# Kernel tuning notes

Measured on AMD Instinct MI355X. Metric: run time of the kernel, lower is better.

Reference implementation:

```python
import jax, jax.numpy as jnp
import numpy as np

B, T, DIM, H, D = 4, 2048, 1024, 8, 128
HDIM = H * D


def _rope_tables(t, head_dim):
    # angular_freq: (1/1024)^linspace(0,1,D/4) concatenated with D/4 zeros -> length D/2
    freq = (1.0 / 1024.0) ** jnp.linspace(0.0, 1.0, head_dim // 4)
    freq = jnp.concatenate([freq.astype(jnp.float32), jnp.zeros(head_dim // 4, jnp.float32)])
    theta = jnp.arange(t, dtype=jnp.float32)[:, None] * freq[None, :]  # [T, D/2]
    return jnp.cos(theta), jnp.sin(theta)


def _rms_norm(x):
    # F.rms_norm with no weight, default eps = finfo(dtype).eps
    eps = jnp.finfo(jnp.float32).eps
    return x * jax.lax.rsqrt(jnp.mean(x * x, axis=-1, keepdims=True) + eps)


def _rope(x, cos, sin):
    # x: [B,T,H,D]; rotate-half form matching the torch module
    x1, x2 = jnp.split(x, 2, axis=-1)
    c = cos[None, :, None, :]
    s = sin[None, :, None, :]
    return jnp.concatenate([x1 * c + x2 * s, -x1 * s + x2 * c], axis=-1)


def setup_inputs() -> dict:
    key = jax.random.key(0)
    k0, k1, k2, k3 = jax.random.split(key, 4)
    std = 0.5 * DIM ** -0.5
    bound = (3.0 ** 0.5) * std
    x = jax.random.normal(k0, (B, T, DIM), jnp.float32)
    ve = jax.random.normal(k1, (B, T, HDIM), jnp.float32)
    qkv_w = jax.random.uniform(k2, (3, HDIM, DIM), jnp.float32, -bound, bound)
    lambdas = jnp.array([0.5, 0.5], jnp.float32)
    # c_proj is zero-initialized in the module; use small random weight so output is nontrivial
    c_proj_w = jax.random.uniform(k3, (DIM, HDIM), jnp.float32, -bound, bound)
    return {"x": x, "ve": ve, "qkv_w": qkv_w, "lambdas": lambdas, "c_proj_w": c_proj_w}


def reference(x, ve, qkv_w, lambdas, c_proj_w):
    b, t, dim = x.shape
    hdim = qkv_w.shape[1]
    h, d = hdim // 128, 128
    # fused QKV projection (no bias)
    qkv = (x @ qkv_w.reshape(3 * hdim, dim).T).reshape(b, t, 3 * h, d)
    q, k, v = qkv[:, :, :h], qkv[:, :, h:2 * h], qkv[:, :, 2 * h:]
    # QK RMSNorm then RoPE
    q, k = _rms_norm(q), _rms_norm(k)
    cos, sin = _rope_tables(t, d)
    q, k = _rope(q, cos, sin), _rope(k, cos, sin)
    # lambda-weighted value-embedding mix
    v = lambdas[0] * v + lambdas[1] * ve.reshape(b, t, h, d)
    # naive attention with explicit causal mask (masked_fill -1e9)
    scores = jnp.einsum('bqhd,bkhd->bhqk', q, k) * (d ** -0.5)
    causal = jnp.triu(jnp.ones((t, t), bool), k=1)  # True above diagonal
    scores = jnp.where(causal[None, None], jnp.float32(-1e9), scores)
    probs = jax.nn.softmax(scores, axis=-1)
    y = jnp.einsum('bhqk,bkhd->bqhd', probs, v).reshape(b, t, hdim)
    return y @ c_proj_w.T
```

## Files before the change

### kernel.cpp

```cpp
#include <hip/hip_runtime.h>
#include <hip/hip_bf16.h>

constexpr int B_ = 4;
constexpr int T_ = 2048;
constexpr int DIM_ = 1024;
constexpr int H_ = 8;
constexpr int D_ = 128;
constexpr int HDIM_ = H_ * D_;

typedef __attribute__((ext_vector_type(8))) short bf16x8;
typedef __attribute__((ext_vector_type(8))) unsigned short ushort8;
typedef __attribute__((ext_vector_type(4))) float f32x4;

#define ATTN_SCALE 0.08838834764831845f

__device__ __forceinline__ unsigned short f2bf(float x) {
    unsigned u = __float_as_uint(x);
    unsigned r = (u + 0x7FFFu + ((u >> 16) & 1u)) >> 16;
    return (unsigned short)r;
}
__device__ __forceinline__ float bf2f(unsigned short u) {
    return __uint_as_float(((unsigned)u) << 16);
}

__device__ __forceinline__ void async_ld16(void* ldsdst, const void* gsrc) {
    __builtin_amdgcn_global_load_lds(
        (const __attribute__((address_space(1))) unsigned int*)gsrc,
        (__attribute__((address_space(3))) unsigned int*)ldsdst, 16, 0, 0);
}

__global__ __launch_bounds__(256) void cvtk(const float* __restrict__ in,
                                            unsigned short* __restrict__ out, int n4) {
    int i = blockIdx.x * 256 + threadIdx.x;
    if (i < n4) {
        float4 v = ((const float4*)in)[i];
        ushort4 o;
        o.x = f2bf(v.x); o.y = f2bf(v.y); o.z = f2bf(v.z); o.w = f2bf(v.w);
        ((ushort4*)out)[i] = o;
    }
}

__global__ void rope_tables_k(float* __restrict__ cost, float* __restrict__ sint) {
    int idx = blockIdx.x * blockDim.x + threadIdx.x;
    if (idx >= T_ * 32) return;
    int t = idx >> 5, j = idx & 31;
    float e = (float)j * (1.0f / 31.0f);
    float freq = powf(1.0f / 1024.0f, e);
    float th = (float)t * freq;
    cost[idx] = cosf(th);
    sint[idx] = sinf(th);
}

__global__ __launch_bounds__(256) void gemm_bf16_nt(
    const unsigned short* __restrict__ A, const unsigned short* __restrict__ Bw,
    float* __restrict__ Cf, unsigned short* __restrict__ Cb,
    int M, int N, int K) {
    __shared__ __align__(16) unsigned short As[128 * 64];
    __shared__ __align__(16) unsigned short Bs[128 * 64];
    const int tid = threadIdx.x;
    const int l = tid & 63, w = tid >> 6;
    const int g = l >> 4, q16 = l & 15;

    int nwg = gridDim.x * gridDim.y;
    int lin = blockIdx.y * gridDim.x + blockIdx.x;
    int swz = (lin & 7) * (nwg >> 3) + (lin >> 3);
    int bx = swz % gridDim.x, by = swz / gridDim.x;
    const size_t m0 = (size_t)by * 128, n0 = (size_t)bx * 128;
    const int wm = (w >> 1) * 64, wn = (w & 1) * 64;

    f32x4 acc[4][4];
#pragma unroll
    for (int i = 0; i < 4; ++i)
#pragma unroll
        for (int j = 0; j < 4; ++j) acc[i][j] = (f32x4){0.f, 0.f, 0.f, 0.f};

    const int srow = l >> 3;
    const int schunk = (l & 7) ^ (srow & 7);
    const unsigned short* aBase = A + (m0 + srow) * (size_t)K + schunk * 8;
    const unsigned short* bBase = Bw + (n0 + srow) * (size_t)K + schunk * 8;
    const int roff = q16 & 7;

    for (int k0 = 0; k0 < K; k0 += 64) {
#pragma unroll
        for (int i = 0; i < 4; ++i) {
            size_t rstep = (size_t)(w * 4 + i) * 8 * K;
            async_ld16(&As[(w * 4 + i) * 512], aBase + rstep + k0);
            async_ld16(&Bs[(w * 4 + i) * 512], bBase + rstep + k0);
        }
        __syncthreads();
        __builtin_amdgcn_s_setprio(1);
#pragma unroll
        for (int ks = 0; ks < 2; ++ks) {
            bf16x8 af[4], bf[4];
#pragma unroll
            for (int f = 0; f < 4; ++f) {
                int off = (ks * 32 + g * 8) ^ (roff << 3);
                af[f] = *(const bf16x8*)&As[(wm + f * 16 + q16) * 64 + off];
                bf[f] = *(const bf16x8*)&Bs[(wn + f * 16 + q16) * 64 + off];
            }
#pragma unroll
            for (int fm = 0; fm < 4; ++fm)
#pragma unroll
                for (int fn = 0; fn < 4; ++fn)
                    acc[fm][fn] = __builtin_amdgcn_mfma_f32_16x16x32_bf16(
                        af[fm], bf[fn], acc[fm][fn], 0, 0, 0);
        }
        __builtin_amdgcn_s_setprio(0);
        __syncthreads();
    }

    if (Cb) {
#pragma unroll
        for (int fm = 0; fm < 4; ++fm)
#pragma unroll
            for (int r = 0; r < 4; ++r) {
                size_t base = (m0 + wm + fm * 16 + 4 * g + r) * (size_t)N + n0 + wn + q16;
#pragma unroll
                for (int fn = 0; fn < 4; ++fn)
                    Cb[base + fn * 16] = f2bf(acc[fm][fn][r]);
            }
    } else {
#pragma unroll
        for (int fm = 0; fm < 4; ++fm)
#pragma unroll
            for (int r = 0; r < 4; ++r) {
                size_t base = (m0 + wm + fm * 16 + 4 * g + r) * (size_t)N + n0 + wn + q16;
#pragma unroll
                for (int fn = 0; fn < 4; ++fn)
                    Cf[base + fn * 16] = acc[fm][fn][r];
            }
    }
}

__global__ __launch_bounds__(256) void qkv_prep_k(
    unsigned short* __restrict__ qkv,
    const float* __restrict__ cost, const float* __restrict__ sint) {
    const int gw = (blockIdx.x * 256 + threadIdx.x) >> 6;
    const int lane = threadIdx.x & 63;
    const int h = gw & (H_ - 1);
    const int t = (gw / H_) & (T_ - 1);
    const int b = gw / (H_ * T_);
    const size_t rowbase = ((size_t)(b * T_ + t) * 3) * HDIM_ + (size_t)h * D_;
    const float c = (lane < 32) ? cost[t * 32 + lane] : 1.0f;
    const float s = (lane < 32) ? sint[t * 32 + lane] : 0.0f;
    const float EPS = 1.1920928955078125e-07f;

#pragma unroll
    for (int qk = 0; qk < 2; ++qk) {
        unsigned short* p = qkv + rowbase + (size_t)qk * HDIM_;
        float x1 = bf2f(p[lane]), x2 = bf2f(p[lane + 64]);
        float ss = x1 * x1 + x2 * x2;
#pragma unroll
        for (int m = 32; m >= 1; m >>= 1) ss += __shfl_xor(ss, m, 64);
        float r = 1.0f / sqrtf(ss * (1.0f / 128.0f) + EPS);
        x1 *= r; x2 *= r;
        p[lane]      = f2bf(x1 * c + x2 * s);
        p[lane + 64] = f2bf(x2 * c - x1 * s);
    }
}

__global__ __launch_bounds__(256) void vtrans_k(
    const unsigned short* __restrict__ qkv, const float* __restrict__ ve,
    const float* __restrict__ lambdas, unsigned short* __restrict__ vT) {
    __shared__ unsigned short lds[64][65];
    const int tid = threadIdx.x;
    const int d0 = blockIdx.x * 64, t0 = blockIdx.y * 64;
    const int p = blockIdx.z;
    const int h = p & 7, b = p >> 3;
    const float l0 = lambdas[0], l1 = lambdas[1];

#pragma unroll
    for (int u = 0; u < 2; ++u) {
        int unit = tid + u * 256;
        int i = unit >> 3, jc = (unit & 7) * 8;
        size_t row = (size_t)(b * T_ + t0 + i);
        ushort8 vv = *(const ushort8*)&qkv[(row * 3 + 2) * HDIM_ + h * D_ + d0 + jc];
        const float* pe = &ve[row * HDIM_ + h * D_ + d0 + jc];
        float4 e0 = *(const float4*)pe;
        float4 e1 = *(const float4*)(pe + 4);
        lds[i][jc + 0] = f2bf(l0 * bf2f(vv[0]) + l1 * e0.x);
        lds[i][jc + 1] = f2bf(l0 * bf2f(vv[1]) + l1 * e0.y);
        lds[i][jc + 2] = f2bf(l0 * bf2f(vv[2]) + l1 * e0.z);
        lds[i][jc + 3] = f2bf(l0 * bf2f(vv[3]) + l1 * e0.w);
        lds[i][jc + 4] = f2bf(l0 * bf2f(vv[4]) + l1 * e1.x);
        lds[i][jc + 5] = f2bf(l0 * bf2f(vv[5]) + l1 * e1.y);
        lds[i][jc + 6] = f2bf(l0 * bf2f(vv[6]) + l1 * e1.z);
        lds[i][jc + 7] = f2bf(l0 * bf2f(vv[7]) + l1 * e1.w);
    }
    __syncthreads();
#pragma unroll
    for (int u = 0; u < 2; ++u) {
        int unit = tid + u * 256;
        int r = unit >> 3, tc = (unit & 7) * 8;
        ushort8 o;
#pragma unroll
        for (int m = 0; m < 8; ++m) o[m] = lds[tc + m][r];
        *(ushort8*)&vT[((size_t)(b * H_ + h) * D_ + d0 + r) * T_ + t0 + tc] = o;
    }
}

__global__ __launch_bounds__(256) void attn_mfma(
    const unsigned short* __restrict__ qkv, const unsigned short* __restrict__ vT,
    unsigned short* __restrict__ y) {
    __shared__ __align__(16) unsigned short Ks[64 * 128];
    __shared__ __align__(16) unsigned short Vs[128 * 64];
    __shared__ __align__(16) unsigned short Pt[4][16 * 64];

    const int tid = threadIdx.x;
    const int l = tid & 63, w = tid >> 6;
    const int g = l >> 4, q16 = l & 15;
    const int bid = blockIdx.x;
    const int xcd = bid & 7, slot = bid >> 3;
    const int pord = slot >> 5, qo = slot & 31;
    const int p = pord * 8 + xcd;
    const int h = p & 7, b = p >> 3;
    const int qt = 31 - qo;
    const int q0 = qt * 64;
    const int roff = q16 & 7;

    const int qrow = q0 + w * 16 + q16;
    const size_t qbase = ((size_t)(b * T_ + qrow) * 3) * HDIM_ + (size_t)h * D_;
    bf16x8 qf[4];
#pragma unroll
    for (int ks = 0; ks < 4; ++ks)
        qf[ks] = *(const bf16x8*)&qkv[qbase + ks * 32 + g * 8];

    f32x4 accO[8];
#pragma unroll
    for (int i = 0; i < 8; ++i) accO[i] = (f32x4){0.f, 0.f, 0.f, 0.f};
    float m_s = -1e30f, l_s = 0.f;

    const int nkv = qt + 1;
    for (int it = 0; it < nkv; ++it) {
        const int kv0 = it * 64;
        __syncthreads();
#pragma unroll
        for (int i = 0; i < 4; ++i) {
            int rloc = (w * 4 + i) * 4 + g;
            int chunk = q16 ^ (rloc & 7);
            const unsigned short* src =
                &qkv[((size_t)(b * T_ + kv0 + rloc) * 3 + 1) * HDIM_ +
                     (size_t)h * D_ + chunk * 8];
            async_ld16(&Ks[(w * 4 + i) * 512], src);
        }
#pragma unroll
        for (int i = 0; i < 4; ++i) {
            int rloc = (w * 4 + i) * 8 + (l >> 3);
            int chunk = (l & 7) ^ (rloc & 7);
            const unsigned short* src =
                &vT[((size_t)(b * H_ + h) * D_ + rloc) * T_ + kv0 + chunk * 8];
            async_ld16(&Vs[(w * 4 + i) * 512], src);
        }
        __syncthreads();

        f32x4 st[4];
        __builtin_amdgcn_s_setprio(1);
#pragma unroll
        for (int fk = 0; fk < 4; ++fk) {
            f32x4 a = (f32x4){0.f, 0.f, 0.f, 0.f};
            int row = fk * 16 + q16;
#pragma unroll
            for (int ks = 0; ks < 4; ++ks) {
                bf16x8 kf = *(const bf16x8*)&Ks[row * 128 +
                                                ((ks * 32 + g * 8) ^ (roff << 3))];
                a = __builtin_amdgcn_mfma_f32_16x16x32_bf16(kf, qf[ks], a, 0, 0, 0);
            }
            st[fk] = a;
        }
        __builtin_amdgcn_s_setprio(0);

        float sv[4][4];
        float pmax = -1e30f;
        const bool edge = (kv0 + 64 > q0);
#pragma unroll
        for (int fk = 0; fk < 4; ++fk)
#pragma unroll
            for (int r = 0; r < 4; ++r) {
                float sc_ = st[fk][r] * ATTN_SCALE;
                if (edge) {
                    int kvg = kv0 + fk * 16 + 4 * g + r;
                    if (kvg > qrow) sc_ = -1e30f;
                }
                sv[fk][r] = sc_;
                pmax = fmaxf(pmax, sc_);
            }
        pmax = fmaxf(pmax, __shfl_xor(pmax, 16));
        pmax = fmaxf(pmax, __shfl_xor(pmax, 32));
        float mnew = fmaxf(m_s, pmax);
        float scl = __expf(m_s - mnew);
        m_s = mnew;
        float rsum = 0.f;
#pragma unroll
        for (int fk = 0; fk < 4; ++fk)
#pragma unroll
            for (int r = 0; r < 4; ++r) {
                sv[fk][r] = __expf(sv[fk][r] - mnew);
                rsum += sv[fk][r];
            }
        rsum += __shfl_xor(rsum, 16);
        rsum += __shfl_xor(rsum, 32);
        l_s = l_s * scl + rsum;

#pragma unroll
        for (int fk = 0; fk < 4; ++fk)
#pragma unroll
            for (int rp = 0; rp < 2; ++rp) {
                unsigned pk = ((unsigned)f2bf(sv[fk][2 * rp + 1]) << 16) |
                              (unsigned)f2bf(sv[fk][2 * rp]);
                int kv = fk * 16 + 4 * g + 2 * rp;
                *(unsigned*)&Pt[w][q16 * 64 + (kv ^ (roff << 3))] = pk;
            }

        f32x4 scv;
        scv[0] = __shfl(scl, 4 * g + 0);
        scv[1] = __shfl(scl, 4 * g + 1);
        scv[2] = __shfl(scl, 4 * g + 2);
        scv[3] = __shfl(scl, 4 * g + 3);
#pragma unroll
        for (int fo = 0; fo < 8; ++fo) accO[fo] *= scv;

        bf16x8 pa[2];
#pragma unroll
        for (int ks = 0; ks < 2; ++ks)
            pa[ks] = *(const bf16x8*)&Pt[w][q16 * 64 + ((ks * 32 + g * 8) ^ (roff << 3))];
        __builtin_amdgcn_s_setprio(1);
#pragma unroll
        for (int fo = 0; fo < 8; ++fo) {
            int drow = fo * 16 + q16;
#pragma unroll
            for (int ks = 0; ks < 2; ++ks) {
                bf16x8 vf = *(const bf16x8*)&Vs[drow * 64 +
                                                ((ks * 32 + g * 8) ^ (roff << 3))];
                accO[fo] = __builtin_amdgcn_mfma_f32_16x16x32_bf16(pa[ks], vf, accO[fo], 0, 0, 0);
            }
        }
        __builtin_amdgcn_s_setprio(0);
    }

    float inv = 1.0f / l_s;
    f32x4 iv;
    iv[0] = __shfl(inv, 4 * g + 0);
    iv[1] = __shfl(inv, 4 * g + 1);
    iv[2] = __shfl(inv, 4 * g + 2);
    iv[3] = __shfl(inv, 4 * g + 3);
#pragma unroll
    for (int r = 0; r < 4; ++r) {
        size_t yb = ((size_t)(b * T_ + q0 + w * 16 + 4 * g + r)) * HDIM_ +
                    (size_t)h * D_ + q16;
#pragma unroll
        for (int fo = 0; fo < 8; ++fo)
            y[yb + fo * 16] = f2bf(accO[fo][r] * iv[r]);
    }
}

extern "C" void kernel_launch(void* const* d_in, const int* in_sizes, int n_in,
                              void* d_out, int out_size, void* d_ws, size_t ws_size,
                              hipStream_t stream) {
    (void)in_sizes; (void)n_in; (void)out_size; (void)ws_size;
    const float* x        = (const float*)d_in[0];
    const float* ve       = (const float*)d_in[1];
    const float* qkv_w    = (const float*)d_in[2];
    const float* lambdas  = (const float*)d_in[3];
    const float* c_proj_w = (const float*)d_in[4];
    float* out = (float*)d_out;

    char* ws = (char*)d_ws;
    unsigned short* qkv = (unsigned short*)ws;
    unsigned short* y   = (unsigned short*)(ws + 50331648);
    unsigned short* xb  = (unsigned short*)(ws + 67108864);
    unsigned short* wb  = (unsigned short*)(ws + 83886080);
    unsigned short* pb  = (unsigned short*)(ws + 90177536);
    float* cost = (float*)(ws + 92274688);
    float* sint = cost + T_ * 32;
    unsigned short* vT  = (unsigned short*)(ws + 100663296);

    hipLaunchKernelGGL(cvtk, dim3(8192), dim3(256), 0, stream, x, xb, 8192 * 1024 / 4);
    hipLaunchKernelGGL(cvtk, dim3(3072), dim3(256), 0, stream, qkv_w, wb, 3072 * 1024 / 4);
    hipLaunchKernelGGL(cvtk, dim3(1024), dim3(256), 0, stream, c_proj_w, pb, 1024 * 1024 / 4);
    hipLaunchKernelGGL(rope_tables_k, dim3(256), dim3(256), 0, stream, cost, sint);

    hipLaunchKernelGGL(gemm_bf16_nt, dim3(24, 64), dim3(256), 0, stream,
                       xb, wb, (float*)nullptr, qkv, B_ * T_, 3 * HDIM_, DIM_);
    hipLaunchKernelGGL(qkv_prep_k, dim3(B_ * T_ * H_ / 4), dim3(256), 0, stream,
                       qkv, cost, sint);
    hipLaunchKernelGGL(vtrans_k, dim3(2, 32, 32), dim3(256), 0, stream,
                       qkv, ve, lambdas, vT);
    hipLaunchKernelGGL(attn_mfma, dim3(1024), dim3(256), 0, stream, qkv, vT, y);
    hipLaunchKernelGGL(gemm_bf16_nt, dim3(8, 64), dim3(256), 0, stream,
                       y, pb, out, (unsigned short*)nullptr, B_ * T_, DIM_, HDIM_);
}
```

Before: 333.6 us.

## Double-buffer KV tiles, widen attention blocks, and add lazy softmax rescaling

The attention kernel now uses 512-thread blocks that each cover 128 query rows, so every staged K/V tile is shared by eight waves instead of four. K/V loads are double-buffered: the next tile is prefetched while the current one is computed, leaving one barrier per iteration. The online softmax skips rescaling the accumulator unless some row's max grows by more than 8, and probabilities are written to LDS as 64-bit stores. The cost is twice the LDS per block and fewer resident blocks, and P values can reach up to e^8 before rescaling, which could slightly affect bf16 accuracy.

Result: no change. 340.2 us (+2.0%).

```diff
diff --git a/kernel.cpp b/kernel.cpp
--- a/kernel.cpp
+++ b/kernel.cpp
@@ -199,24 +199,47 @@
     }
 }
 
-__global__ __launch_bounds__(256) void attn_mfma(
+__global__ __launch_bounds__(512, 4) void attn_mfma(
     const unsigned short* __restrict__ qkv, const unsigned short* __restrict__ vT,
     unsigned short* __restrict__ y) {
-    __shared__ __align__(16) unsigned short Ks[64 * 128];
-    __shared__ __align__(16) unsigned short Vs[128 * 64];
-    __shared__ __align__(16) unsigned short Pt[4][16 * 64];
+    __shared__ __align__(16) unsigned short Ks[2][64 * 128];
+    __shared__ __align__(16) unsigned short Vs[2][128 * 64];
+    __shared__ __align__(16) unsigned short Pt[8][16 * 64];
 
     const int tid = threadIdx.x;
     const int l = tid & 63, w = tid >> 6;
     const int g = l >> 4, q16 = l & 15;
     const int bid = blockIdx.x;
     const int xcd = bid & 7, slot = bid >> 3;
-    const int pord = slot >> 5, qo = slot & 31;
+    const int pord = slot >> 4, qo = slot & 15;
     const int p = pord * 8 + xcd;
     const int h = p & 7, b = p >> 3;
-    const int qt = 31 - qo;
-    const int q0 = qt * 64;
+    const int qt = 15 - qo;
+    const int q0 = qt * 128;
     const int roff = q16 & 7;
+
+    const int jk0 = w * 2;
+    const int krow0 = jk0 * 4 + g,        krow1 = (jk0 + 1) * 4 + g;
+    const int kch0  = q16 ^ (krow0 & 7),  kch1  = q16 ^ (krow1 & 7);
+    const int vrow0 = jk0 * 8 + (l >> 3), vrow1 = (jk0 + 1) * 8 + (l >> 3);
+    const int vch0  = (l & 7) ^ (vrow0 & 7), vch1 = (l & 7) ^ (vrow1 & 7);
+    const unsigned short* kp0 =
+        &qkv[((size_t)(b * T_ + krow0) * 3 + 1) * HDIM_ + h * D_ + kch0 * 8];
+    const unsigned short* kp1 =
+        &qkv[((size_t)(b * T_ + krow1) * 3 + 1) * HDIM_ + h * D_ + kch1 * 8];
+    const unsigned short* vp0 =
+        &vT[((size_t)(b * H_ + h) * D_ + vrow0) * T_ + vch0 * 8];
+    const unsigned short* vp1 =
+        &vT[((size_t)(b * H_ + h) * D_ + vrow1) * T_ + vch1 * 8];
+    const size_t kstep = (size_t)64 * 3 * HDIM_;
+
+#define STAGE_KV(buf, it_) do {                                   \
+        size_t ko_ = (size_t)(it_) * kstep; int vo_ = (it_) * 64; \
+        async_ld16(&Ks[buf][jk0 * 512],       kp0 + ko_);         \
+        async_ld16(&Ks[buf][(jk0 + 1) * 512], kp1 + ko_);         \
+        async_ld16(&Vs[buf][jk0 * 512],       vp0 + vo_);         \
+        async_ld16(&Vs[buf][(jk0 + 1) * 512], vp1 + vo_);         \
+    } while (0)
 
     const int qrow = q0 + w * 16 + q16;
     const size_t qbase = ((size_t)(b * T_ + qrow) * 3) * HDIM_ + (size_t)h * D_;
@@ -230,28 +253,14 @@
     for (int i = 0; i < 8; ++i) accO[i] = (f32x4){0.f, 0.f, 0.f, 0.f};
     float m_s = -1e30f, l_s = 0.f;
 
-    const int nkv = qt + 1;
+    const int nkv = 2 * qt + 2;
+    int cur = 0;
+    STAGE_KV(0, 0);
+
     for (int it = 0; it < nkv; ++it) {
         const int kv0 = it * 64;
         __syncthreads();
-#pragma unroll
-        for (int i = 0; i < 4; ++i) {
-            int rloc = (w * 4 + i) * 4 + g;
-            int chunk = q16 ^ (rloc & 7);
-            const unsigned short* src =
-                &qkv[((size_t)(b * T_ + kv0 + rloc) * 3 + 1) * HDIM_ +
-                     (size_t)h * D_ + chunk * 8];
-            async_ld16(&Ks[(w * 4 + i) * 512], src);
-        }
-#pragma unroll
-        for (int i = 0; i < 4; ++i) {
-            int rloc = (w * 4 + i) * 8 + (l >> 3);
-            int chunk = (l & 7) ^ (rloc & 7);
-            const unsigned short* src =
-                &vT[((size_t)(b * H_ + h) * D_ + rloc) * T_ + kv0 + chunk * 8];
-            async_ld16(&Vs[(w * 4 + i) * 512], src);
-        }
-        __syncthreads();
+        if (it + 1 < nkv) STAGE_KV(cur ^ 1, it + 1);
 
         f32x4 st[4];
         __builtin_amdgcn_s_setprio(1);
@@ -261,7 +270,7 @@
             int row = fk * 16 + q16;
 #pragma unroll
             for (int ks = 0; ks < 4; ++ks) {
-                bf16x8 kf = *(const bf16x8*)&Ks[row * 128 +
+                bf16x8 kf = *(const bf16x8*)&Ks[cur][row * 128 +
                                                 ((ks * 32 + g * 8) ^ (roff << 3))];
                 a = __builtin_amdgcn_mfma_f32_16x16x32_bf16(kf, qf[ks], a, 0, 0, 0);
             }
@@ -286,38 +295,43 @@
             }
         pmax = fmaxf(pmax, __shfl_xor(pmax, 16));
         pmax = fmaxf(pmax, __shfl_xor(pmax, 32));
-        float mnew = fmaxf(m_s, pmax);
-        float scl = __expf(m_s - mnew);
-        m_s = mnew;
+
+        if (!__all(pmax - m_s <= 8.0f)) {
+            float mnew = fmaxf(m_s, pmax);
+            float scl = __expf(m_s - mnew);
+            m_s = mnew;
+            l_s *= scl;
+            f32x4 scv;
+            scv[0] = __shfl(scl, 4 * g + 0);
+            scv[1] = __shfl(scl, 4 * g + 1);
+            scv[2] = __shfl(scl, 4 * g + 2);
+            scv[3] = __shfl(scl, 4 * g + 3);
+#pragma unroll
+            for (int fo = 0; fo < 8; ++fo) accO[fo] *= scv;
+        }
+
         float rsum = 0.f;
 #pragma unroll
         for (int fk = 0; fk < 4; ++fk)
 #pragma unroll
             for (int r = 0; r < 4; ++r) {
-                sv[fk][r] = __expf(sv[fk][r] - mnew);
+                sv[fk][r] = __expf(sv[fk][r] - m_s);
                 rsum += sv[fk][r];
             }
         rsum += __shfl_xor(rsum, 16);
         rsum += __shfl_xor(rsum, 32);
-        l_s = l_s * scl + rsum;
-
-#pragma unroll
-        for (int fk = 0; fk < 4; ++fk)
-#pragma unroll
-            for (int rp = 0; rp < 2; ++rp) {
-                unsigned pk = ((unsigned)f2bf(sv[fk][2 * rp + 1]) << 16) |
-                              (unsigned)f2bf(sv[fk][2 * rp]);
-                int kv = fk * 16 + 4 * g + 2 * rp;
-                *(unsigned*)&Pt[w][q16 * 64 + (kv ^ (roff << 3))] = pk;
-            }
-
-        f32x4 scv;
-        scv[0] = __shfl(scl, 4 * g + 0);
-        scv[1] = __shfl(scl, 4 * g + 1);
-        scv[2] = __shfl(scl, 4 * g + 2);
-        scv[3] = __shfl(scl, 4 * g + 3);
-#pragma unroll
-        for (int fo = 0; fo < 8; ++fo) accO[fo] *= scv;
+        l_s += rsum;
+
+#pragma unroll
+        for (int fk = 0; fk < 4; ++fk) {
+            unsigned long long pk =
+                (unsigned long long)f2bf(sv[fk][0])        |
+                ((unsigned long long)f2bf(sv[fk][1]) << 16) |
+                ((unsigned long long)f2bf(sv[fk][2]) << 32) |
+                ((unsigned long long)f2bf(sv[fk][3]) << 48);
+            int kv = fk * 16 + 4 * g;
+            *(unsigned long long*)&Pt[w][q16 * 64 + (kv ^ (roff << 3))] = pk;
+        }
 
         bf16x8 pa[2];
 #pragma unroll
@@ -329,13 +343,15 @@
             int drow = fo * 16 + q16;
 #pragma unroll
             for (int ks = 0; ks < 2; ++ks) {
-                bf16x8 vf = *(const bf16x8*)&Vs[drow * 64 +
+                bf16x8 vf = *(const bf16x8*)&Vs[cur][drow * 64 +
                                                 ((ks * 32 + g * 8) ^ (roff << 3))];
                 accO[fo] = __builtin_amdgcn_mfma_f32_16x16x32_bf16(pa[ks], vf, accO[fo], 0, 0, 0);
             }
         }
         __builtin_amdgcn_s_setprio(0);
-    }
+        cur ^= 1;
+    }
+#undef STAGE_KV
 
     float inv = 1.0f / l_s;
     f32x4 iv;
@@ -385,7 +401,7 @@
                        qkv, cost, sint);
     hipLaunchKernelGGL(vtrans_k, dim3(2, 32, 32), dim3(256), 0, stream,
                        qkv, ve, lambdas, vT);
-    hipLaunchKernelGGL(attn_mfma, dim3(1024), dim3(256), 0, stream, qkv, vT, y);
+    hipLaunchKernelGGL(attn_mfma, dim3(512), dim3(512), 0, stream, qkv, vT, y);
     hipLaunchKernelGGL(gemm_bf16_nt, dim3(8, 64), dim3(256), 0, stream,
                        y, pb, out, (unsigned short*)nullptr, B_ * T_, DIM_, HDIM_);
 }
```
